# Kernel optimization log

Hardware: AMD Instinct MI355X
Metric: run time of the kernel (lower is better)

## Reference

```python
import jax, jax.numpy as jnp
import numpy as np

B, C, H, W = 2, 512, 48, 48
HEADS = 8
REDUCTION = 4
DPH = max(C // REDUCTION // HEADS, 1)   # 16
TOTAL = DPH * HEADS                      # 128
EPS_NORM = 1e-12
EPS_BN = 1e-5


def setup_inputs() -> dict:
    key = jax.random.key(0)
    ks = jax.random.split(key, 6)
    x = jax.random.normal(ks[0], (B, C, H, W), dtype=jnp.float32)
    # 1x1 convs stored as [out_ch, in_ch] matrices
    w_qkv = jax.random.normal(ks[1], (3 * TOTAL, C), dtype=jnp.float32) * (1.0 / np.sqrt(C))
    w_out = jax.random.normal(ks[2], (C, TOTAL), dtype=jnp.float32) * (1.0 / np.sqrt(TOTAL))
    temperature = jnp.ones((HEADS, 1, 1), dtype=jnp.float32)
    bn_gamma = jnp.ones((C,), dtype=jnp.float32)
    bn_beta = jnp.zeros((C,), dtype=jnp.float32)
    return {"x": x, "w_qkv": w_qkv, "temperature": temperature,
            "w_out": w_out, "bn_gamma": bn_gamma, "bn_beta": bn_beta}


def _l2norm(t):
    # F.normalize(t, dim=-1): t / max(||t||_2, eps)
    n = jnp.sqrt(jnp.sum(t * t, axis=-1, keepdims=True))
    return t / jnp.maximum(n, EPS_NORM)


def reference(x, w_qkv, temperature, w_out, bn_gamma, bn_beta):
    b, c, h, w = x.shape
    n = h * w
    # qkv 1x1 conv: [b, 3*TOTAL, h, w]
    qkv = jnp.einsum('bchw,oc->bohw', x, w_qkv)
    q, k, v = jnp.split(qkv, 3, axis=1)
    # [b, heads, dph, n] -> [b, heads, n, dph]
    def heads_tokens(t):
        return t.reshape(b, HEADS, DPH, n).transpose(0, 1, 3, 2)
    q = _l2norm(heads_tokens(q))
    k = _l2norm(heads_tokens(k))
    v = heads_tokens(v)
    # [b, heads, n, n]
    attn = jnp.einsum('bhnd,bhmd->bhnm', q, k) * temperature[None]
    attn = jax.nn.softmax(attn, axis=-1)
    out = jnp.einsum('bhnm,bhmd->bhnd', attn, v)          # [b, heads, n, dph]
    out = out.transpose(0, 1, 3, 2).reshape(b, TOTAL, h, w)
    # project_out: 1x1 conv then BatchNorm2d (training-mode batch stats)
    out = jnp.einsum('bthw,ct->bchw', out, w_out)
    mean = jnp.mean(out, axis=(0, 2, 3))
    var = jnp.mean((out - mean[None, :, None, None]) ** 2, axis=(0, 2, 3))
    out = (out - mean[None, :, None, None]) * jax.lax.rsqrt(var + EPS_BN)[None, :, None, None]
    out = out * bn_gamma[None, :, None, None] + bn_beta[None, :, None, None]
    return out
```

## Files before the change

### kernel.cpp

```cpp
#include <hip/hip_runtime.h>

#define NB 2
#define CC 512
#define NN 2304
#define NH 8
#define DD 16
#define TT 128
#define O3 384

typedef __attribute__((ext_vector_type(4))) float f32x4;
typedef __attribute__((ext_vector_type(8))) __bf16 bf16x8;
typedef __attribute__((ext_vector_type(4))) __bf16 bf16x4;
typedef __attribute__((ext_vector_type(4))) _Float16 f16x4;

__global__ __launch_bounds__(256) void k0_convert(
    const float* __restrict__ x, const float* __restrict__ wqkv,
    const float* __restrict__ wout,
    __bf16* __restrict__ xT, __bf16* __restrict__ wqb, __bf16* __restrict__ wob)
{
    int bid = blockIdx.x;
    int t = threadIdx.x;
    if (bid < 576) {
        __shared__ float tile[64][65];
        int b = bid / 288, rem = bid % 288;
        int nt = rem / 8, cb = rem % 8;
        int n0 = nt * 64, c0 = cb * 64;
        int tc = t >> 6, tn = t & 63;
#pragma unroll
        for (int i = 0; i < 16; i++) {
            int cl = i * 4 + tc;
            tile[cl][tn] = x[(size_t)(b * CC + c0 + cl) * NN + n0 + tn];
        }
        __syncthreads();
#pragma unroll
        for (int i = 0; i < 16; i++) {
            int nl = i * 4 + tc;
            xT[(size_t)(b * NN + n0 + nl) * CC + c0 + tn] = (__bf16)tile[tn][nl];
        }
    } else {
        int wid = bid - 576;
        int base = wid * 256 + t;
#pragma unroll
        for (int i = 0; i < 16; i++) {
            int j = base + i * 16384;
            if (j < O3 * CC) wqb[j] = (__bf16)wqkv[j];
            else             wob[j - O3 * CC] = (__bf16)wout[j - O3 * CC];
        }
    }
}

__global__ __launch_bounds__(256) void k1_qkv(
    const __bf16* __restrict__ xT, const __bf16* __restrict__ wqb,
    _Float16* __restrict__ Q, _Float16* __restrict__ K, _Float16* __restrict__ VT)
{
    int ob = blockIdx.x, nt = blockIdx.y, b = blockIdx.z;
    int lane = threadIdx.x & 63, wave = threadIdx.x >> 6;
    int quad = lane >> 4, col = lane & 15;
    int n0 = nt * 64 + wave * 16;
    int o0 = ob * 32;

    f32x4 acc[2];
    acc[0] = (f32x4){0.f, 0.f, 0.f, 0.f};
    acc[1] = (f32x4){0.f, 0.f, 0.f, 0.f};

    const __bf16* arow = xT + (size_t)(b * NN + n0 + col) * CC + quad * 8;
    const __bf16* brow0 = wqb + (size_t)(o0 + col) * CC + quad * 8;
    const __bf16* brow1 = brow0 + 16 * CC;

    bf16x8 a  = *(const bf16x8*)(arow);
    bf16x8 w0 = *(const bf16x8*)(brow0);
    bf16x8 w1 = *(const bf16x8*)(brow1);
#pragma unroll
    for (int ks = 0; ks < 16; ks++) {
        bf16x8 an, wn0, wn1;
        if (ks < 15) {
            an  = *(const bf16x8*)(arow + (ks + 1) * 32);
            wn0 = *(const bf16x8*)(brow0 + (ks + 1) * 32);
            wn1 = *(const bf16x8*)(brow1 + (ks + 1) * 32);
        }
        acc[0] = __builtin_amdgcn_mfma_f32_16x16x32_bf16(a, w0, acc[0], 0, 0, 0);
        acc[1] = __builtin_amdgcn_mfma_f32_16x16x32_bf16(a, w1, acc[1], 0, 0, 0);
        a = an; w0 = wn0; w1 = wn1;
    }

#pragma unroll
    for (int s = 0; s < 2; s++) {
        int oc = o0 + s * 16 + col;
        int d = oc & 15, h = (oc >> 4) & 7, kind = oc >> 7;
        f32x4 v = acc[s];
        if (kind < 2) {
            float ss0 = v[0] * v[0], ss1 = v[1] * v[1], ss2 = v[2] * v[2], ss3 = v[3] * v[3];
#pragma unroll
            for (int m = 1; m < 16; m <<= 1) {
                ss0 += __shfl_xor(ss0, m);
                ss1 += __shfl_xor(ss1, m);
                ss2 += __shfl_xor(ss2, m);
                ss3 += __shfl_xor(ss3, m);
            }
            v[0] *= 1.0f / fmaxf(sqrtf(ss0), 1e-12f);
            v[1] *= 1.0f / fmaxf(sqrtf(ss1), 1e-12f);
            v[2] *= 1.0f / fmaxf(sqrtf(ss2), 1e-12f);
            v[3] *= 1.0f / fmaxf(sqrtf(ss3), 1e-12f);
            _Float16* dst = (kind == 0 ? Q : K) + (size_t)(b * NH + h) * NN * DD;
#pragma unroll
            for (int r = 0; r < 4; r++) {
                int n = n0 + quad * 4 + r;
                dst[(size_t)n * DD + d] = (_Float16)v[r];
            }
        } else {
            f16x4 pk;
#pragma unroll
            for (int r = 0; r < 4; r++) pk[r] = (_Float16)v[r];
            int n = n0 + quad * 4;
            *(f16x4*)(VT + (size_t)((b * NH + h) * DD + d) * NN + n) = pk;
        }
    }
}

__global__ __launch_bounds__(512) void k2_attn(
    const _Float16* __restrict__ Q, const _Float16* __restrict__ K,
    const _Float16* __restrict__ VT, const float* __restrict__ temp,
    __bf16* __restrict__ AO)
{
    __shared__ float Osh[8][16][64];
    __shared__ float Lsh[8][64];

    int qt = blockIdx.x, bh = blockIdx.y;
    int lane = threadIdx.x & 63, wave = threadIdx.x >> 6;
    int quad = lane >> 4, col = lane & 15;
    int kbase = wave * 288;
    int qbase = qt * 64;

    const _Float16* Qb = Q + (size_t)bh * NN * DD;
    float tl2 = temp[bh & 7] * 1.4426950408889634f;

    f16x4 qf0 = *(const f16x4*)(Qb + (size_t)(qbase +  0 + col) * DD + quad * 4);
    f16x4 qf1 = *(const f16x4*)(Qb + (size_t)(qbase + 16 + col) * DD + quad * 4);
    f16x4 qf2 = *(const f16x4*)(Qb + (size_t)(qbase + 32 + col) * DD + quad * 4);
    f16x4 qf3 = *(const f16x4*)(Qb + (size_t)(qbase + 48 + col) * DD + quad * 4);

    f32x4 oa0 = {0.f,0.f,0.f,0.f}, oa1 = {0.f,0.f,0.f,0.f};
    f32x4 oa2 = {0.f,0.f,0.f,0.f}, oa3 = {0.f,0.f,0.f,0.f};
    float la0 = 0.f, la1 = 0.f, la2 = 0.f, la3 = 0.f;
    const f32x4 zc = {0.f,0.f,0.f,0.f};

    const _Float16* kp = K + (size_t)bh * NN * DD + (size_t)(kbase + col) * DD + quad * 4;
    const _Float16* vp = VT + (size_t)bh * DD * NN + (size_t)col * NN + kbase + quad * 4;

    f16x4 kfa = *(const f16x4*)(kp);
    f16x4 kfb = *(const f16x4*)(kp + 16 * DD);
    f16x4 vfa = *(const f16x4*)(vp);
    f16x4 vfb = *(const f16x4*)(vp + 16);

#define K2_CHUNK(KF, VF)                                                        \
    {                                                                           \
        f32x4 s0 = __builtin_amdgcn_mfma_f32_16x16x16f16(KF, qf0, zc, 0, 0, 0); \
        f32x4 s1 = __builtin_amdgcn_mfma_f32_16x16x16f16(KF, qf1, zc, 0, 0, 0); \
        f32x4 s2 = __builtin_amdgcn_mfma_f32_16x16x16f16(KF, qf2, zc, 0, 0, 0); \
        f32x4 s3 = __builtin_amdgcn_mfma_f32_16x16x16f16(KF, qf3, zc, 0, 0, 0); \
        f16x4 p0, p1, p2, p3;                                                   \
        _Pragma("unroll")                                                       \
        for (int r = 0; r < 4; ++r) {                                           \
            float e0 = __builtin_amdgcn_exp2f(tl2 * s0[r]);                     \
            float e1 = __builtin_amdgcn_exp2f(tl2 * s1[r]);                     \
            float e2 = __builtin_amdgcn_exp2f(tl2 * s2[r]);                     \
            float e3 = __builtin_amdgcn_exp2f(tl2 * s3[r]);                     \
            p0[r] = (_Float16)e0; la0 += e0;                                    \
            p1[r] = (_Float16)e1; la1 += e1;                                    \
            p2[r] = (_Float16)e2; la2 += e2;                                    \
            p3[r] = (_Float16)e3; la3 += e3;                                    \
        }                                                                       \
        oa0 = __builtin_amdgcn_mfma_f32_16x16x16f16(VF, p0, oa0, 0, 0, 0);      \
        oa1 = __builtin_amdgcn_mfma_f32_16x16x16f16(VF, p1, oa1, 0, 0, 0);      \
        oa2 = __builtin_amdgcn_mfma_f32_16x16x16f16(VF, p2, oa2, 0, 0, 0);      \
        oa3 = __builtin_amdgcn_mfma_f32_16x16x16f16(VF, p3, oa3, 0, 0, 0);      \
    }

    for (int g = 0; g < 9; ++g) {
        f16x4 kna, knb, vna, vnb;
        if (g < 8) {
            kna = *(const f16x4*)(kp + 32 * DD);
            knb = *(const f16x4*)(kp + 48 * DD);
            vna = *(const f16x4*)(vp + 32);
            vnb = *(const f16x4*)(vp + 48);
        }
        K2_CHUNK(kfa, vfa)
        K2_CHUNK(kfb, vfb)
        kfa = kna; kfb = knb; vfa = vna; vfb = vnb;
        kp += 32 * DD; vp += 32;
    }
#undef K2_CHUNK

    la0 += __shfl_xor(la0, 16); la0 += __shfl_xor(la0, 32);
    la1 += __shfl_xor(la1, 16); la1 += __shfl_xor(la1, 32);
    la2 += __shfl_xor(la2, 16); la2 += __shfl_xor(la2, 32);
    la3 += __shfl_xor(la3, 16); la3 += __shfl_xor(la3, 32);

#pragma unroll
    for (int r = 0; r < 4; ++r) {
        Osh[wave][quad * 4 + r][ 0 + col] = oa0[r];
        Osh[wave][quad * 4 + r][16 + col] = oa1[r];
        Osh[wave][quad * 4 + r][32 + col] = oa2[r];
        Osh[wave][quad * 4 + r][48 + col] = oa3[r];
    }
    float lv = (quad == 0) ? la0 : (quad == 1) ? la1 : (quad == 2) ? la2 : la3;
    Lsh[wave][quad * 16 + col] = lv;
    __syncthreads();

    int t = threadIdx.x;
    int q = t & 63, dg = t >> 6;
    float l = 0.f;
#pragma unroll
    for (int w = 0; w < 8; ++w) l += Lsh[w][q];
    float inv = 1.0f / l;
    float o0 = 0.f, o1 = 0.f;
#pragma unroll
    for (int w = 0; w < 8; ++w) {
        o0 += Osh[w][dg * 2 + 0][q];
        o1 += Osh[w][dg * 2 + 1][q];
    }
    int b = bh >> 3, h = bh & 7;
    __bf16* dst = AO + (size_t)(b * NN + qbase + q) * TT + h * DD + dg * 2;
    dst[0] = (__bf16)(o0 * inv);
    dst[1] = (__bf16)(o1 * inv);
}

__global__ __launch_bounds__(256) void k3_proj(
    const __bf16* __restrict__ AO, const __bf16* __restrict__ wob,
    float* __restrict__ out)
{
    int cb = blockIdx.x, nt = blockIdx.y, b = blockIdx.z;
    int lane = threadIdx.x & 63, wave = threadIdx.x >> 6;
    int quad = lane >> 4, col = lane & 15;
    int n0 = nt * 64 + wave * 16, c0 = cb * 32;

    f32x4 acc[2];
    acc[0] = (f32x4){0.f, 0.f, 0.f, 0.f};
    acc[1] = (f32x4){0.f, 0.f, 0.f, 0.f};

    const __bf16* ab = AO + (size_t)(b * NN + n0 + col) * TT + quad * 8;
    const __bf16* wb0 = wob + (size_t)(c0 + col) * TT + quad * 8;
    const __bf16* wb1 = wb0 + 16 * TT;
#pragma unroll
    for (int ks = 0; ks < 4; ks++) {
        bf16x8 a  = *(const bf16x8*)(ab + ks * 32);
        bf16x8 w0 = *(const bf16x8*)(wb0 + ks * 32);
        bf16x8 w1 = *(const bf16x8*)(wb1 + ks * 32);
        acc[0] = __builtin_amdgcn_mfma_f32_16x16x32_bf16(a, w0, acc[0], 0, 0, 0);
        acc[1] = __builtin_amdgcn_mfma_f32_16x16x32_bf16(a, w1, acc[1], 0, 0, 0);
    }
#pragma unroll
    for (int s = 0; s < 2; s++) {
        int c = c0 + s * 16 + col;
        float* dst = out + (size_t)(b * CC + c) * NN + n0 + quad * 4;
        *(f32x4*)dst = acc[s];
    }
}

__global__ __launch_bounds__(256) void k4_bn(
    float* __restrict__ out, const float* __restrict__ gamma,
    const float* __restrict__ beta)
{
    int c = blockIdx.x;
    int t = threadIdx.x;
    float vals[18];
    float s = 0.f, q = 0.f;
#pragma unroll
    for (int i = 0; i < 18; i++) {
        int j = i * 256 + t;
        int b = j / NN, n = j % NN;
        float v = out[(size_t)(b * CC + c) * NN + n];
        vals[i] = v; s += v; q += v * v;
    }
#pragma unroll
    for (int m = 1; m < 64; m <<= 1) { s += __shfl_xor(s, m); q += __shfl_xor(q, m); }
    __shared__ float rs[4], rq[4];
    int lane = t & 63, wave = t >> 6;
    if (lane == 0) { rs[wave] = s; rq[wave] = q; }
    __syncthreads();
    s = rs[0] + rs[1] + rs[2] + rs[3];
    q = rq[0] + rq[1] + rq[2] + rq[3];
    float mean = s * (1.0f / 4608.0f);
    float var = q * (1.0f / 4608.0f) - mean * mean;
    float sc = rsqrtf(var + 1e-5f) * gamma[c];
    float sh = beta[c] - mean * sc;
#pragma unroll
    for (int i = 0; i < 18; i++) {
        int j = i * 256 + t;
        int b = j / NN, n = j % NN;
        out[(size_t)(b * CC + c) * NN + n] = vals[i] * sc + sh;
    }
}

extern "C" void kernel_launch(void* const* d_in, const int* in_sizes, int n_in,
                              void* d_out, int out_size, void* d_ws, size_t ws_size,
                              hipStream_t stream) {
    const float* x     = (const float*)d_in[0];
    const float* wqkv  = (const float*)d_in[1];
    const float* temp  = (const float*)d_in[2];
    const float* wout  = (const float*)d_in[3];
    const float* gamma = (const float*)d_in[4];
    const float* beta  = (const float*)d_in[5];
    float* out = (float*)d_out;

    char* ws = (char*)d_ws;
    const size_t OFF_XT = 0;
    const size_t OFF_WQ = 4718592;
    const size_t OFF_WO = 5111808;
    const size_t OFF_Q  = 5242880;
    const size_t OFF_K  = 6422528;
    const size_t OFF_VT = 7602176;
    const size_t OFF_AO = 8781824;

    __bf16* xT  = (__bf16*)(ws + OFF_XT);
    __bf16* wqb = (__bf16*)(ws + OFF_WQ);
    __bf16* wob = (__bf16*)(ws + OFF_WO);
    _Float16* Q  = (_Float16*)(ws + OFF_Q);
    _Float16* K  = (_Float16*)(ws + OFF_K);
    _Float16* VT = (_Float16*)(ws + OFF_VT);
    __bf16* AO  = (__bf16*)(ws + OFF_AO);

    k0_convert<<<640, 256, 0, stream>>>(x, wqkv, wout, xT, wqb, wob);
    k1_qkv<<<dim3(12, 36, 2), 256, 0, stream>>>(xT, wqb, Q, K, VT);
    k2_attn<<<dim3(36, 16), 512, 0, stream>>>(Q, K, VT, temp, AO);
    k3_proj<<<dim3(16, 36, 2), 256, 0, stream>>>(AO, wob, out);
    k4_bn<<<512, 256, 0, stream>>>(out, gamma, beta);
}
```

Before: 138.2 us.

## Fold temperature into Q, pack exp with cvt_pkrtz, MFMA row sums, widen QKV tile

The attention kernel pre-scales the Q fragments by temperature*log2e in fp16, which removes a per-score multiply. It converts exponentials to half pairs with the packed round-toward-zero instruction and computes the softmax denominators with an extra MFMA against a ones vector instead of scalar adds and cross-lane shuffles. The QKV GEMM kernel now computes 64 output channels per block instead of 32, halving its grid and reusing each A fragment across four MFMAs. The trade-offs are more MFMA work in the attention loop, lower precision for the scaled Q and the rounded row sums, and fewer blocks in k1.

```diff
diff --git a/kernel.cpp b/kernel.cpp
--- a/kernel.cpp
+++ b/kernel.cpp
@@ -12,6 +12,20 @@
 typedef __attribute__((ext_vector_type(8))) __bf16 bf16x8;
 typedef __attribute__((ext_vector_type(4))) __bf16 bf16x4;
 typedef __attribute__((ext_vector_type(4))) _Float16 f16x4;
+typedef __attribute__((ext_vector_type(2))) __fp16 hf16x2;
+
+union hf2pair {
+    hf16x2 h[2];
+    f16x4  v;
+};
+
+#define OFF_XT 0u
+#define OFF_WQ 4718592u
+#define OFF_WO 5111808u
+#define OFF_Q  5242880u
+#define OFF_K  6422528u
+#define OFF_VT 7602176u
+#define OFF_AO 8781824u
 
 __global__ __launch_bounds__(256) void k0_convert(
     const float* __restrict__ x, const float* __restrict__ wqkv,
@@ -57,37 +71,44 @@
     int lane = threadIdx.x & 63, wave = threadIdx.x >> 6;
     int quad = lane >> 4, col = lane & 15;
     int n0 = nt * 64 + wave * 16;
-    int o0 = ob * 32;
-
-    f32x4 acc[2];
-    acc[0] = (f32x4){0.f, 0.f, 0.f, 0.f};
-    acc[1] = (f32x4){0.f, 0.f, 0.f, 0.f};
-
-    const __bf16* arow = xT + (size_t)(b * NN + n0 + col) * CC + quad * 8;
+    int o0 = ob * 64;
+
+    f32x4 acc0 = {0.f,0.f,0.f,0.f}, acc1 = {0.f,0.f,0.f,0.f};
+    f32x4 acc2 = {0.f,0.f,0.f,0.f}, acc3 = {0.f,0.f,0.f,0.f};
+
+    const __bf16* arow  = xT + (size_t)(b * NN + n0 + col) * CC + quad * 8;
     const __bf16* brow0 = wqb + (size_t)(o0 + col) * CC + quad * 8;
     const __bf16* brow1 = brow0 + 16 * CC;
+    const __bf16* brow2 = brow0 + 32 * CC;
+    const __bf16* brow3 = brow0 + 48 * CC;
 
     bf16x8 a  = *(const bf16x8*)(arow);
     bf16x8 w0 = *(const bf16x8*)(brow0);
     bf16x8 w1 = *(const bf16x8*)(brow1);
+    bf16x8 w2 = *(const bf16x8*)(brow2);
+    bf16x8 w3 = *(const bf16x8*)(brow3);
 #pragma unroll
     for (int ks = 0; ks < 16; ks++) {
-        bf16x8 an, wn0, wn1;
+        bf16x8 an, wn0, wn1, wn2, wn3;
         if (ks < 15) {
             an  = *(const bf16x8*)(arow + (ks + 1) * 32);
             wn0 = *(const bf16x8*)(brow0 + (ks + 1) * 32);
             wn1 = *(const bf16x8*)(brow1 + (ks + 1) * 32);
-        }
-        acc[0] = __builtin_amdgcn_mfma_f32_16x16x32_bf16(a, w0, acc[0], 0, 0, 0);
-        acc[1] = __builtin_amdgcn_mfma_f32_16x16x32_bf16(a, w1, acc[1], 0, 0, 0);
-        a = an; w0 = wn0; w1 = wn1;
-    }
-
-#pragma unroll
-    for (int s = 0; s < 2; s++) {
+            wn2 = *(const bf16x8*)(brow2 + (ks + 1) * 32);
+            wn3 = *(const bf16x8*)(brow3 + (ks + 1) * 32);
+        }
+        acc0 = __builtin_amdgcn_mfma_f32_16x16x32_bf16(a, w0, acc0, 0, 0, 0);
+        acc1 = __builtin_amdgcn_mfma_f32_16x16x32_bf16(a, w1, acc1, 0, 0, 0);
+        acc2 = __builtin_amdgcn_mfma_f32_16x16x32_bf16(a, w2, acc2, 0, 0, 0);
+        acc3 = __builtin_amdgcn_mfma_f32_16x16x32_bf16(a, w3, acc3, 0, 0, 0);
+        a = an; w0 = wn0; w1 = wn1; w2 = wn2; w3 = wn3;
+    }
+
+#pragma unroll
+    for (int s = 0; s < 4; s++) {
         int oc = o0 + s * 16 + col;
         int d = oc & 15, h = (oc >> 4) & 7, kind = oc >> 7;
-        f32x4 v = acc[s];
+        f32x4 v = (s == 0) ? acc0 : (s == 1) ? acc1 : (s == 2) ? acc2 : acc3;
         if (kind < 2) {
             float ss0 = v[0] * v[0], ss1 = v[1] * v[1], ss2 = v[2] * v[2], ss3 = v[3] * v[3];
 #pragma unroll
@@ -133,15 +154,22 @@
 
     const _Float16* Qb = Q + (size_t)bh * NN * DD;
     float tl2 = temp[bh & 7] * 1.4426950408889634f;
+    _Float16 tl2h = (_Float16)tl2;
 
     f16x4 qf0 = *(const f16x4*)(Qb + (size_t)(qbase +  0 + col) * DD + quad * 4);
     f16x4 qf1 = *(const f16x4*)(Qb + (size_t)(qbase + 16 + col) * DD + quad * 4);
     f16x4 qf2 = *(const f16x4*)(Qb + (size_t)(qbase + 32 + col) * DD + quad * 4);
     f16x4 qf3 = *(const f16x4*)(Qb + (size_t)(qbase + 48 + col) * DD + quad * 4);
+#pragma unroll
+    for (int j = 0; j < 4; j++) {
+        qf0[j] *= tl2h; qf1[j] *= tl2h; qf2[j] *= tl2h; qf3[j] *= tl2h;
+    }
+    const f16x4 onesf = {(_Float16)1.f, (_Float16)1.f, (_Float16)1.f, (_Float16)1.f};
 
     f32x4 oa0 = {0.f,0.f,0.f,0.f}, oa1 = {0.f,0.f,0.f,0.f};
     f32x4 oa2 = {0.f,0.f,0.f,0.f}, oa3 = {0.f,0.f,0.f,0.f};
-    float la0 = 0.f, la1 = 0.f, la2 = 0.f, la3 = 0.f;
+    f32x4 lc0 = {0.f,0.f,0.f,0.f}, lc1 = {0.f,0.f,0.f,0.f};
+    f32x4 lc2 = {0.f,0.f,0.f,0.f}, lc3 = {0.f,0.f,0.f,0.f};
     const f32x4 zc = {0.f,0.f,0.f,0.f};
 
     const _Float16* kp = K + (size_t)bh * NN * DD + (size_t)(kbase + col) * DD + quad * 4;
@@ -158,18 +186,28 @@
         f32x4 s1 = __builtin_amdgcn_mfma_f32_16x16x16f16(KF, qf1, zc, 0, 0, 0); \
         f32x4 s2 = __builtin_amdgcn_mfma_f32_16x16x16f16(KF, qf2, zc, 0, 0, 0); \
         f32x4 s3 = __builtin_amdgcn_mfma_f32_16x16x16f16(KF, qf3, zc, 0, 0, 0); \
-        f16x4 p0, p1, p2, p3;                                                   \
-        _Pragma("unroll")                                                       \
-        for (int r = 0; r < 4; ++r) {                                           \
-            float e0 = __builtin_amdgcn_exp2f(tl2 * s0[r]);                     \
-            float e1 = __builtin_amdgcn_exp2f(tl2 * s1[r]);                     \
-            float e2 = __builtin_amdgcn_exp2f(tl2 * s2[r]);                     \
-            float e3 = __builtin_amdgcn_exp2f(tl2 * s3[r]);                     \
-            p0[r] = (_Float16)e0; la0 += e0;                                    \
-            p1[r] = (_Float16)e1; la1 += e1;                                    \
-            p2[r] = (_Float16)e2; la2 += e2;                                    \
-            p3[r] = (_Float16)e3; la3 += e3;                                    \
-        }                                                                       \
+        hf2pair u0, u1, u2, u3;                                                 \
+        u0.h[0] = __builtin_amdgcn_cvt_pkrtz(__builtin_amdgcn_exp2f(s0[0]),     \
+                                             __builtin_amdgcn_exp2f(s0[1]));    \
+        u0.h[1] = __builtin_amdgcn_cvt_pkrtz(__builtin_amdgcn_exp2f(s0[2]),     \
+                                             __builtin_amdgcn_exp2f(s0[3]));    \
+        u1.h[0] = __builtin_amdgcn_cvt_pkrtz(__builtin_amdgcn_exp2f(s1[0]),     \
+                                             __builtin_amdgcn_exp2f(s1[1]));    \
+        u1.h[1] = __builtin_amdgcn_cvt_pkrtz(__builtin_amdgcn_exp2f(s1[2]),     \
+                                             __builtin_amdgcn_exp2f(s1[3]));    \
+        u2.h[0] = __builtin_amdgcn_cvt_pkrtz(__builtin_amdgcn_exp2f(s2[0]),     \
+                                             __builtin_amdgcn_exp2f(s2[1]));    \
+        u2.h[1] = __builtin_amdgcn_cvt_pkrtz(__builtin_amdgcn_exp2f(s2[2]),     \
+                                             __builtin_amdgcn_exp2f(s2[3]));    \
+        u3.h[0] = __builtin_amdgcn_cvt_pkrtz(__builtin_amdgcn_exp2f(s3[0]),     \
+                                             __builtin_amdgcn_exp2f(s3[1]));    \
+        u3.h[1] = __builtin_amdgcn_cvt_pkrtz(__builtin_amdgcn_exp2f(s3[2]),     \
+                                             __builtin_amdgcn_exp2f(s3[3]));    \
+        f16x4 p0 = u0.v, p1 = u1.v, p2 = u2.v, p3 = u3.v;                       \
+        lc0 = __builtin_amdgcn_mfma_f32_16x16x16f16(onesf, p0, lc0, 0, 0, 0);   \
+        lc1 = __builtin_amdgcn_mfma_f32_16x16x16f16(onesf, p1, lc1, 0, 0, 0);   \
+        lc2 = __builtin_amdgcn_mfma_f32_16x16x16f16(onesf, p2, lc2, 0, 0, 0);   \
+        lc3 = __builtin_amdgcn_mfma_f32_16x16x16f16(onesf, p3, lc3, 0, 0, 0);   \
         oa0 = __builtin_amdgcn_mfma_f32_16x16x16f16(VF, p0, oa0, 0, 0, 0);      \
         oa1 = __builtin_amdgcn_mfma_f32_16x16x16f16(VF, p1, oa1, 0, 0, 0);      \
         oa2 = __builtin_amdgcn_mfma_f32_16x16x16f16(VF, p2, oa2, 0, 0, 0);      \
@@ -191,11 +229,6 @@
     }
 #undef K2_CHUNK
 
-    la0 += __shfl_xor(la0, 16); la0 += __shfl_xor(la0, 32);
-    la1 += __shfl_xor(la1, 16); la1 += __shfl_xor(la1, 32);
-    la2 += __shfl_xor(la2, 16); la2 += __shfl_xor(la2, 32);
-    la3 += __shfl_xor(la3, 16); la3 += __shfl_xor(la3, 32);
-
 #pragma unroll
     for (int r = 0; r < 4; ++r) {
         Osh[wave][quad * 4 + r][ 0 + col] = oa0[r];
@@ -203,7 +236,7 @@
         Osh[wave][quad * 4 + r][32 + col] = oa2[r];
         Osh[wave][quad * 4 + r][48 + col] = oa3[r];
     }
-    float lv = (quad == 0) ? la0 : (quad == 1) ? la1 : (quad == 2) ? la2 : la3;
+    float lv = (quad == 0) ? lc0[0] : (quad == 1) ? lc1[0] : (quad == 2) ? lc2[0] : lc3[0];
     Lsh[wave][quad * 16 + col] = lv;
     __syncthreads();
 
@@ -234,9 +267,8 @@
     int quad = lane >> 4, col = lane & 15;
     int n0 = nt * 64 + wave * 16, c0 = cb * 32;
 
-    f32x4 acc[2];
-    acc[0] = (f32x4){0.f, 0.f, 0.f, 0.f};
-    acc[1] = (f32x4){0.f, 0.f, 0.f, 0.f};
+    f32x4 acc0 = {0.f, 0.f, 0.f, 0.f};
+    f32x4 acc1 = {0.f, 0.f, 0.f, 0.f};
 
     const __bf16* ab = AO + (size_t)(b * NN + n0 + col) * TT + quad * 8;
     const __bf16* wb0 = wob + (size_t)(c0 + col) * TT + quad * 8;
@@ -246,14 +278,14 @@
         bf16x8 a  = *(const bf16x8*)(ab + ks * 32);
         bf16x8 w0 = *(const bf16x8*)(wb0 + ks * 32);
         bf16x8 w1 = *(const bf16x8*)(wb1 + ks * 32);
-        acc[0] = __builtin_amdgcn_mfma_f32_16x16x32_bf16(a, w0, acc[0], 0, 0, 0);
-        acc[1] = __builtin_amdgcn_mfma_f32_16x16x32_bf16(a, w1, acc[1], 0, 0, 0);
+        acc0 = __builtin_amdgcn_mfma_f32_16x16x32_bf16(a, w0, acc0, 0, 0, 0);
+        acc1 = __builtin_amdgcn_mfma_f32_16x16x32_bf16(a, w1, acc1, 0, 0, 0);
     }
 #pragma unroll
     for (int s = 0; s < 2; s++) {
         int c = c0 + s * 16 + col;
         float* dst = out + (size_t)(b * CC + c) * NN + n0 + quad * 4;
-        *(f32x4*)dst = acc[s];
+        *(f32x4*)dst = (s == 0) ? acc0 : acc1;
     }
 }
 
@@ -302,15 +334,7 @@
     const float* gamma = (const float*)d_in[4];
     const float* beta  = (const float*)d_in[5];
     float* out = (float*)d_out;
-
     char* ws = (char*)d_ws;
-    const size_t OFF_XT = 0;
-    const size_t OFF_WQ = 4718592;
-    const size_t OFF_WO = 5111808;
-    const size_t OFF_Q  = 5242880;
-    const size_t OFF_K  = 6422528;
-    const size_t OFF_VT = 7602176;
-    const size_t OFF_AO = 8781824;
 
     __bf16* xT  = (__bf16*)(ws + OFF_XT);
     __bf16* wqb = (__bf16*)(ws + OFF_WQ);
@@ -321,7 +345,7 @@
     __bf16* AO  = (__bf16*)(ws + OFF_AO);
 
     k0_convert<<<640, 256, 0, stream>>>(x, wqkv, wout, xT, wqb, wob);
-    k1_qkv<<<dim3(12, 36, 2), 256, 0, stream>>>(xT, wqb, Q, K, VT);
+    k1_qkv<<<dim3(6, 36, 2), 256, 0, stream>>>(xT, wqb, Q, K, VT);
     k2_attn<<<dim3(36, 16), 512, 0, stream>>>(Q, K, VT, temp, AO);
     k3_proj<<<dim3(16, 36, 2), 256, 0, stream>>>(AO, wob, out);
     k4_bn<<<512, 256, 0, stream>>>(out, gamma, beta);
```

Measured after the change: 134.1 us. 1.03x faster.
